# Optimization experiments

Measured on AMD Instinct MI355X. Metric: run time of the kernel, lower is better.

Reference implementation:

```python
import jax, jax.numpy as jnp
import numpy as np

B, T, C, H = 2, 2048, 1024, 16
HS = C // H  # head_size = 64
EPS = 1e-5


def setup_inputs() -> dict:
    key = jax.random.key(0)
    ks = jax.random.split(key, 12)
    s = 0.02
    return {
        "x": jax.random.normal(ks[0], (B, T, C), jnp.float32),
        # per-head q/k/v linears stacked on a leading head axis [H, C, HS]
        "Wq": jax.random.normal(ks[1], (H, C, HS), jnp.float32) * s,
        "bq": jnp.zeros((H, HS), jnp.float32),
        "Wk": jax.random.normal(ks[2], (H, C, HS), jnp.float32) * s,
        "bk": jnp.zeros((H, HS), jnp.float32),
        "Wv": jax.random.normal(ks[3], (H, C, HS), jnp.float32) * s,
        "bv": jnp.zeros((H, HS), jnp.float32),
        # output projection [H*HS, C] == [C, C]
        "Wo": jax.random.normal(ks[4], (C, C), jnp.float32) * s,
        "bo": jnp.zeros((C,), jnp.float32),
        # feed-forward: C -> 4C -> C
        "W1": jax.random.normal(ks[5], (C, 4 * C), jnp.float32) * s,
        "b1": jnp.zeros((4 * C,), jnp.float32),
        "W2": jax.random.normal(ks[6], (4 * C, C), jnp.float32) * s,
        "b2": jnp.zeros((C,), jnp.float32),
        # custom LayerNorm params (broadcast over last dim)
        "gamma1": jnp.ones((C,), jnp.float32),
        "beta1": jnp.zeros((C,), jnp.float32),
        "gamma2": jnp.ones((C,), jnp.float32),
        "beta2": jnp.zeros((C,), jnp.float32),
    }


def _ln(x, gamma, beta):
    # NOTE: faithful to the source: normalizes over axis=1 (the SEQUENCE axis
    # for [B,T,C] input), uses unbiased variance (torch default), and puts eps
    # OUTSIDE the sqrt: (x - mean) / (sqrt(var) + eps).
    mean = x.mean(axis=1, keepdims=True)
    var = x.var(axis=1, keepdims=True, ddof=1)
    return gamma * ((x - mean) / (jnp.sqrt(var) + EPS)) + beta


def reference(x, Wq, bq, Wk, bk, Wv, bv, Wo, bo, W1, b1, W2, b2,
              gamma1, beta1, gamma2, beta2):
    # --- self-attention sublayer (pre-norm, residual) ---
    h = _ln(x, gamma1, beta1)
    q = jnp.einsum('btc,hcd->bhtd', h, Wq) + bq[None, :, None, :]
    k = jnp.einsum('btc,hcd->bhtd', h, Wk) + bk[None, :, None, :]
    v = jnp.einsum('btc,hcd->bhtd', h, Wv) + bv[None, :, None, :]
    wei = jax.nn.softmax(jnp.einsum('bhtd,bhsd->bhts', q, k) * (HS ** -0.5), axis=-1)
    attn = jnp.einsum('bhts,bhsd->bhtd', wei, v)          # [B,H,T,HS]
    attn = attn.transpose(0, 2, 1, 3).reshape(B, T, H * HS)  # head-order concat
    x = x + attn @ Wo + bo
    # --- feed-forward sublayer (pre-norm, residual) ---
    h2 = _ln(x, gamma2, beta2)
    x = x + jax.nn.relu(h2 @ W1 + b1) @ W2 + b2
    return x
```

## Files before the change

kernel.cpp:

```cpp
#include <hip/hip_runtime.h>
#include <hip/hip_bf16.h>

#define Bq 2
#define Tq 2048
#define Cq 1024
#define Hq 16
#define HSq 64
#define EPSq 1e-5f

using bf16 = __hip_bfloat16;
using f32x4 = __attribute__((ext_vector_type(4))) float;
using f32x16 = __attribute__((ext_vector_type(16))) float;
using bf16x8 = __attribute__((ext_vector_type(8))) __bf16;

__device__ __forceinline__ bf16 f2bf(float f) { return __float2bfloat16(f); }
__device__ __forceinline__ unsigned short f2u(float f) {
    return __builtin_bit_cast(unsigned short, __float2bfloat16(f));
}
__device__ __forceinline__ void gload16(const void* g, void* l) {
    __builtin_amdgcn_global_load_lds((const __attribute__((address_space(1))) void*)g,
                                     (__attribute__((address_space(3))) void*)l, 16, 0, 0);
}

__global__ void k_transpose(const float* __restrict__ src, bf16* __restrict__ dst,
                            int R, int Cc, long strideSrc, long strideDst) {
    __shared__ bf16 tile[32][33];
    const long zb = blockIdx.z;
    src += zb * strideSrc;
    dst += zb * strideDst;
    int c0 = blockIdx.x * 32, r0 = blockIdx.y * 32;
    int tx = threadIdx.x & 31, ty = threadIdx.x >> 5;
    for (int i = ty; i < 32; i += 8)
        tile[i][tx] = f2bf(src[(long)(r0 + i) * Cc + (c0 + tx)]);
    __syncthreads();
    for (int i = ty; i < 32; i += 8)
        dst[(long)(c0 + i) * R + (r0 + tx)] = tile[tx][i];
}

__global__ void k_pack_bias(const float* __restrict__ a, const float* __restrict__ b,
                            const float* __restrict__ c, float* __restrict__ dst) {
    int i = blockIdx.x * 256 + threadIdx.x;
    dst[i] = a[i];
    dst[1024 + i] = b[i];
    dst[2048 + i] = c[i];
}

__global__ void k_ln_part(const float* __restrict__ x, float* __restrict__ ps,
                          float* __restrict__ pss) {
    int c = blockIdx.x * 256 + threadIdx.x;
    int b = blockIdx.y;
    int tc = blockIdx.z;
    const float* p = x + (long)b * Tq * Cq + (long)tc * 64 * Cq + c;
    float s = 0.f, ss = 0.f;
    for (int t = 0; t < 64; ++t) {
        float v = p[(long)t * Cq];
        s += v;
        ss += v * v;
    }
    long o = ((long)tc * Bq + b) * Cq + c;
    ps[o] = s;
    pss[o] = ss;
}

__global__ void k_ln_fin(const float* __restrict__ ps, const float* __restrict__ pss,
                         float* __restrict__ mean, float* __restrict__ rstd) {
    int i = blockIdx.x * 256 + threadIdx.x;
    float s = 0.f, ss = 0.f;
    for (int tc = 0; tc < 32; ++tc) {
        s += ps[(long)tc * (Bq * Cq) + i];
        ss += pss[(long)tc * (Bq * Cq) + i];
    }
    float m = s / (float)Tq;
    float var = (ss - s * m) / (float)(Tq - 1);
    var = fmaxf(var, 0.f);
    mean[i] = m;
    rstd[i] = 1.0f / (sqrtf(var) + EPSq);
}

__global__ void k_ln_apply(const float* __restrict__ x, const float* __restrict__ mean,
                           const float* __restrict__ rstd, const float* __restrict__ gamma,
                           const float* __restrict__ beta, bf16* __restrict__ out) {
    long i = (long)blockIdx.x * 256 + threadIdx.x;
    int c = (int)(i & (Cq - 1));
    long bt = i >> 10;
    int b = (int)(bt >> 11);
    float m = mean[b * Cq + c], r = rstd[b * Cq + c];
    out[i] = f2bf(gamma[c] * ((x[i] - m) * r) + beta[c]);
}

__device__ __forceinline__ void xcd_swizzle(int& bx, int& by) {
    const int gx = gridDim.x;
    const int nwg = gx * gridDim.y;
    const int bid = blockIdx.y * gx + blockIdx.x;
    const int swz = (bid & 7) * (nwg >> 3) + (bid >> 3);
    bx = swz % gx;
    by = swz / gx;
}

template <int MODE>
__global__ __launch_bounds__(256, 3) void k_gemm_nt(
    const bf16* __restrict__ A, int lda, const bf16* __restrict__ Bt, int ldb, int K,
    const float* __restrict__ bias, bf16* __restrict__ outB, int ldout) {
    __shared__ __bf16 sA[2][128 * 32];
    __shared__ __bf16 sB[2][128 * 32];
    int bx, by;
    xcd_swizzle(bx, by);
    const int m0 = by * 128, n0 = bx * 128;
    const int tid = threadIdx.x;
    const int lane = tid & 63, wave = tid >> 6;
    const int lane15 = lane & 15, quad = lane >> 4;
    const int wm = (wave >> 1) * 64, wn = (wave & 1) * 64;
    const int srow = wave * 16 + (lane >> 2);
    const int scol = (((lane & 3) ^ ((lane >> 3) & 3)) * 8);
    const int sq8 = (quad ^ ((lane15 >> 1) & 3)) * 8;
    __bf16* a00 = &sA[0][wave * 512];
    __bf16* a01 = &sA[0][2048 + wave * 512];
    __bf16* a10 = &sA[1][wave * 512];
    __bf16* a11 = &sA[1][2048 + wave * 512];
    __bf16* b00 = &sB[0][wave * 512];
    __bf16* b01 = &sB[0][2048 + wave * 512];
    __bf16* b10 = &sB[1][wave * 512];
    __bf16* b11 = &sB[1][2048 + wave * 512];
    const bf16* Ap = A + (long)(m0 + srow) * lda + scol;
    const bf16* Ap2 = Ap + 64L * lda;
    const bf16* Bp = Bt + (long)(n0 + srow) * ldb + scol;
    const bf16* Bp2 = Bp + 64L * ldb;

    f32x4 acc[4][4];
#pragma unroll
    for (int i = 0; i < 4; ++i)
#pragma unroll
        for (int j = 0; j < 4; ++j)
#pragma unroll
            for (int p = 0; p < 4; ++p) acc[i][j][p] = 0.f;

    for (int k0 = 0; k0 < K; k0 += 64) {
        __syncthreads();
        gload16(Ap + k0, a00);
        gload16(Ap2 + k0, a01);
        gload16(Ap + k0 + 32, a10);
        gload16(Ap2 + k0 + 32, a11);
        gload16(Bp + k0, b00);
        gload16(Bp2 + k0, b01);
        gload16(Bp + k0 + 32, b10);
        gload16(Bp2 + k0 + 32, b11);
        __syncthreads();
#pragma unroll
        for (int kk = 0; kk < 2; ++kk) {
            bf16x8 af[4], bfr[4];
#pragma unroll
            for (int i = 0; i < 4; ++i)
                af[i] = *(const bf16x8*)(&sA[kk][(wm + i * 16 + lane15) * 32 + sq8]);
#pragma unroll
            for (int j = 0; j < 4; ++j)
                bfr[j] = *(const bf16x8*)(&sB[kk][(wn + j * 16 + lane15) * 32 + sq8]);
#pragma unroll
            for (int i = 0; i < 4; ++i)
#pragma unroll
                for (int j = 0; j < 4; ++j)
                    acc[i][j] = __builtin_amdgcn_mfma_f32_16x16x32_bf16(af[i], bfr[j],
                                                                        acc[i][j], 0, 0, 0);
        }
    }
    if (MODE == 0) {
#pragma unroll
        for (int i = 0; i < 4; ++i) {
            const int mm = m0 + wm + i * 16 + quad * 4;
            const int b = mm >> 11, t4 = mm & (Tq - 1);
#pragma unroll
            for (int j = 0; j < 4; ++j) {
                const int n = n0 + wn + j * 16 + lane15;
                const int which = n >> 10, hh = (n >> 6) & (Hq - 1), d = n & (HSq - 1);
                const long bh = (long)b * Hq + hh;
                const float bb = bias[n];
                if (which == 0) {
#pragma unroll
                    for (int p = 0; p < 4; ++p)
                        outB[bh * 131072 + (long)(t4 + p) * HSq + d] =
                            f2bf((acc[i][j][p] + bb) * 0.125f);
                } else if (which == 1) {
#pragma unroll
                    for (int p = 0; p < 4; ++p)
                        outB[4194304L + bh * 131072 + (long)(t4 + p) * HSq + d] =
                            f2bf(acc[i][j][p] + bb);
                } else {
                    ushort4 pk;
                    pk.x = f2u(acc[i][j][0] + bb);
                    pk.y = f2u(acc[i][j][1] + bb);
                    pk.z = f2u(acc[i][j][2] + bb);
                    pk.w = f2u(acc[i][j][3] + bb);
                    *(ushort4*)(&outB[8388608L + bh * 131072 + (long)d * Tq + t4]) = pk;
                }
            }
        }
    } else {
#pragma unroll
        for (int i = 0; i < 4; ++i) {
#pragma unroll
            for (int p = 0; p < 4; ++p) {
                const int m = m0 + wm + i * 16 + quad * 4 + p;
#pragma unroll
                for (int j = 0; j < 4; ++j) {
                    const int n = n0 + wn + j * 16 + lane15;
                    outB[(long)m * ldout + n] = f2bf(fmaxf(acc[i][j][p] + bias[n], 0.f));
                }
            }
        }
    }
}

template <int MODE>
__global__ __launch_bounds__(256, 4) void k_gemm_n64(
    const bf16* __restrict__ A, int lda, const bf16* __restrict__ Bt, int ldb, int K,
    const float* __restrict__ bias, const float* __restrict__ residF,
    float* __restrict__ outF, int ldout) {
    __shared__ __bf16 sA[2][128 * 32];
    __shared__ __bf16 sB[2][64 * 32];
    int bx, by;
    xcd_swizzle(bx, by);
    const int m0 = by * 128, n0 = bx * 64;
    const int tid = threadIdx.x;
    const int lane = tid & 63, wave = tid >> 6;
    const int lane15 = lane & 15, quad = lane >> 4;
    const int wm = wave * 32;
    const int srow = wave * 16 + (lane >> 2);
    const int scol = (((lane & 3) ^ ((lane >> 3) & 3)) * 8);
    const int sq8 = (quad ^ ((lane15 >> 1) & 3)) * 8;
    __bf16* a00 = &sA[0][wave * 512];
    __bf16* a01 = &sA[0][2048 + wave * 512];
    __bf16* a10 = &sA[1][wave * 512];
    __bf16* a11 = &sA[1][2048 + wave * 512];
    __bf16* b00 = &sB[0][wave * 512];
    __bf16* b10 = &sB[1][wave * 512];
    const bf16* Ap = A + (long)(m0 + srow) * lda + scol;
    const bf16* Ap2 = Ap + 64L * lda;
    const bf16* Bp = Bt + (long)(n0 + srow) * ldb + scol;

    f32x4 acc[2][4];
#pragma unroll
    for (int i = 0; i < 2; ++i)
#pragma unroll
        for (int j = 0; j < 4; ++j)
#pragma unroll
            for (int p = 0; p < 4; ++p) acc[i][j][p] = 0.f;

    for (int k0 = 0; k0 < K; k0 += 64) {
        __syncthreads();
        gload16(Ap + k0, a00);
        gload16(Ap2 + k0, a01);
        gload16(Ap + k0 + 32, a10);
        gload16(Ap2 + k0 + 32, a11);
        gload16(Bp + k0, b00);
        gload16(Bp + k0 + 32, b10);
        __syncthreads();
#pragma unroll
        for (int kk = 0; kk < 2; ++kk) {
            bf16x8 af[2], bfr[4];
#pragma unroll
            for (int i = 0; i < 2; ++i)
                af[i] = *(const bf16x8*)(&sA[kk][(wm + i * 16 + lane15) * 32 + sq8]);
#pragma unroll
            for (int j = 0; j < 4; ++j)
                bfr[j] = *(const bf16x8*)(&sB[kk][(j * 16 + lane15) * 32 + sq8]);
#pragma unroll
            for (int i = 0; i < 2; ++i)
#pragma unroll
                for (int j = 0; j < 4; ++j)
                    acc[i][j] = __builtin_amdgcn_mfma_f32_16x16x32_bf16(af[i], bfr[j],
                                                                        acc[i][j], 0, 0, 0);
        }
    }
#pragma unroll
    for (int i = 0; i < 2; ++i) {
#pragma unroll
        for (int p = 0; p < 4; ++p) {
            const int m = m0 + wm + i * 16 + quad * 4 + p;
#pragma unroll
            for (int j = 0; j < 4; ++j) {
                const int n = n0 + j * 16 + lane15;
                outF[(long)m * ldout + n] =
                    acc[i][j][p] + bias[n] + residF[(long)m * ldout + n];
            }
        }
    }
}

__global__ __launch_bounds__(256, 2) void k_attn(const bf16* __restrict__ qkv,
                                                 bf16* __restrict__ attn) {
    __shared__ __bf16 sK[64 * 72];
    __shared__ __bf16 sVt[64 * 72];
    const int bh = blockIdx.y;
    const int q0 = blockIdx.x * 128;
    const int tid = threadIdx.x, wave = tid >> 6, lane = tid & 63;
    const int lane31 = lane & 31, laneh = lane >> 5;
    const bf16* Qp = qkv + (long)bh * 131072;
    const bf16* Kp = qkv + 4194304L + (long)bh * 131072;
    const bf16* Vtp = qkv + 8388608L + (long)bh * 131072;
    bf16x8 qa[4];
#pragma unroll
    for (int s = 0; s < 4; ++s)
        qa[s] = *(const bf16x8*)(&Qp[(long)(q0 + wave * 32 + lane31) * HSq + s * 16 + laneh * 8]);
    f32x16 o[2];
#pragma unroll
    for (int dt = 0; dt < 2; ++dt)
#pragma unroll
        for (int r = 0; r < 16; ++r) o[dt][r] = 0.f;
    float rs = 0.f;
    const int r0 = tid >> 3, c0 = (tid & 7) * 8;
    const int r1 = r0 + 32;

    uint4 nk0 = *(const uint4*)(&Kp[(long)r0 * HSq + c0]);
    uint4 nk1 = *(const uint4*)(&Kp[(long)r1 * HSq + c0]);
    uint4 nv0 = *(const uint4*)(&Vtp[(long)r0 * Tq + c0]);
    uint4 nv1 = *(const uint4*)(&Vtp[(long)r1 * Tq + c0]);

    for (int kc = 0; kc < Tq; kc += 64) {
        __syncthreads();
        *(uint4*)(&sK[r0 * 72 + c0]) = nk0;
        *(uint4*)(&sK[r1 * 72 + c0]) = nk1;
        *(uint4*)(&sVt[r0 * 72 + c0]) = nv0;
        *(uint4*)(&sVt[r1 * 72 + c0]) = nv1;
        __syncthreads();
        if (kc + 64 < Tq) {
            nk0 = *(const uint4*)(&Kp[(long)(kc + 64 + r0) * HSq + c0]);
            nk1 = *(const uint4*)(&Kp[(long)(kc + 64 + r1) * HSq + c0]);
            nv0 = *(const uint4*)(&Vtp[(long)r0 * Tq + kc + 64 + c0]);
            nv1 = *(const uint4*)(&Vtp[(long)r1 * Tq + kc + 64 + c0]);
        }
#pragma unroll
        for (int nt = 0; nt < 2; ++nt) {
            f32x16 z;
#pragma unroll
            for (int r = 0; r < 16; ++r) z[r] = 0.f;
            __builtin_amdgcn_s_setprio(1);
#pragma unroll
            for (int s = 0; s < 4; ++s) {
                bf16x8 kb =
                    *(const bf16x8*)(&sK[(nt * 32 + lane31) * 72 + s * 16 + laneh * 8]);
                z = __builtin_amdgcn_mfma_f32_32x32x16_bf16(kb, qa[s], z, 0, 0, 0);
            }
            __builtin_amdgcn_s_setprio(0);
            float e[16];
#pragma unroll
            for (int r = 0; r < 16; ++r) {
                e[r] = __expf(z[r]);
                rs += e[r];
            }
            unsigned int pk[8];
#pragma unroll
            for (int g = 0; g < 4; ++g)
#pragma unroll
                for (int h = 0; h < 2; ++h)
                    pk[g * 2 + h] = (unsigned int)f2u(e[g * 4 + 2 * h]) |
                                    ((unsigned int)f2u(e[g * 4 + 2 * h + 1]) << 16);
            unsigned int sa0 = laneh ? pk[0] : pk[2], sa1 = laneh ? pk[1] : pk[3];
            unsigned int ra0 = __shfl_xor((int)sa0, 32), ra1 = __shfl_xor((int)sa1, 32);
            unsigned int sb0 = laneh ? pk[4] : pk[6], sb1 = laneh ? pk[5] : pk[7];
            unsigned int rb0 = __shfl_xor((int)sb0, 32), rb1 = __shfl_xor((int)sb1, 32);
            uint4 f0, f1;
            if (laneh == 0) {
                f0 = {pk[0], pk[1], ra0, ra1};
                f1 = {pk[4], pk[5], rb0, rb1};
            } else {
                f0 = {ra0, ra1, pk[2], pk[3]};
                f1 = {rb0, rb1, pk[6], pk[7]};
            }
            bf16x8 pa0 = __builtin_bit_cast(bf16x8, f0);
            bf16x8 pa1 = __builtin_bit_cast(bf16x8, f1);
            __builtin_amdgcn_s_setprio(1);
#pragma unroll
            for (int dt = 0; dt < 2; ++dt) {
                bf16x8 vb0 =
                    *(const bf16x8*)(&sVt[(dt * 32 + lane31) * 72 + nt * 32 + laneh * 8]);
                bf16x8 vb1 = *(const bf16x8*)(&sVt[(dt * 32 + lane31) * 72 + nt * 32 + 16 +
                                                   laneh * 8]);
                o[dt] = __builtin_amdgcn_mfma_f32_32x32x16_bf16(pa0, vb0, o[dt], 0, 0, 0);
                o[dt] = __builtin_amdgcn_mfma_f32_32x32x16_bf16(pa1, vb1, o[dt], 0, 0, 0);
            }
            __builtin_amdgcn_s_setprio(0);
        }
    }
    float ltot = rs + __shfl_xor(rs, 32);
    float linv = 1.0f / ltot;
    const int b = bh >> 4, hh = bh & 15;
#pragma unroll
    for (int r = 0; r < 16; ++r) {
        const int tl = (r & 3) + 8 * (r >> 2) + 4 * laneh;
        float inv = __shfl(linv, tl);
        const int t = q0 + wave * 32 + tl;
        const long base = ((long)b * Tq + t) * Cq + hh * HSq;
#pragma unroll
        for (int dt = 0; dt < 2; ++dt)
            attn[base + dt * 32 + lane31] = f2bf(o[dt][r] * inv);
    }
}

extern "C" void kernel_launch(void* const* d_in, const int* in_sizes, int n_in,
                              void* d_out, int out_size, void* d_ws, size_t ws_size,
                              hipStream_t stream) {
    const float* x = (const float*)d_in[0];
    const float* Wq = (const float*)d_in[1];
    const float* bqv = (const float*)d_in[2];
    const float* Wk = (const float*)d_in[3];
    const float* bkv = (const float*)d_in[4];
    const float* Wv = (const float*)d_in[5];
    const float* bvv = (const float*)d_in[6];
    const float* Wo = (const float*)d_in[7];
    const float* bo = (const float*)d_in[8];
    const float* W1 = (const float*)d_in[9];
    const float* b1 = (const float*)d_in[10];
    const float* W2 = (const float*)d_in[11];
    const float* b2 = (const float*)d_in[12];
    const float* g1 = (const float*)d_in[13];
    const float* be1 = (const float*)d_in[14];
    const float* g2 = (const float*)d_in[15];
    const float* be2 = (const float*)d_in[16];

    char* ws = (char*)d_ws;
    size_t off = 0;
    auto alloc = [&](size_t bytes) {
        void* p = ws + off;
        off += (bytes + 255) & ~(size_t)255;
        return p;
    };
    bf16* regA = (bf16*)alloc(32L * 1024 * 1024);
    float* x2 = (float*)alloc(4096L * 1024 * 4);
    bf16* buf1 = (bf16*)alloc(4096L * 1024 * 2);
    float* bqkv = (float*)alloc(3072L * 4);
    float* ps = (float*)alloc(32L * Bq * Cq * 4);
    float* pss = (float*)alloc(32L * Bq * Cq * 4);
    float* mean1 = (float*)alloc(Bq * Cq * 4);
    float* rstd1 = (float*)alloc(Bq * Cq * 4);
    float* mean2 = (float*)alloc(Bq * Cq * 4);
    float* rstd2 = (float*)alloc(Bq * Cq * 4);
    bf16* dres = (bf16*)d_out;
    float* outF = (float*)d_out;

    k_ln_part<<<dim3(4, Bq, 32), 256, 0, stream>>>(x, ps, pss);
    k_ln_fin<<<dim3(8), 256, 0, stream>>>(ps, pss, mean1, rstd1);
    k_ln_apply<<<dim3(16384), 256, 0, stream>>>(x, mean1, rstd1, g1, be1, dres);

    k_transpose<<<dim3(2, 32, 16), 256, 0, stream>>>(Wq, buf1, 1024, 64, 65536, 65536);
    k_transpose<<<dim3(2, 32, 16), 256, 0, stream>>>(Wk, buf1 + 1048576, 1024, 64, 65536, 65536);
    k_transpose<<<dim3(2, 32, 16), 256, 0, stream>>>(Wv, buf1 + 2097152, 1024, 64, 65536, 65536);
    k_pack_bias<<<dim3(4), 256, 0, stream>>>(bqv, bkv, bvv, bqkv);
    k_gemm_nt<0><<<dim3(24, 32), 256, 0, stream>>>(dres, 1024, buf1, 1024, 1024, bqkv, regA, 0);
    k_attn<<<dim3(16, 32), 256, 0, stream>>>(regA, dres);
    k_transpose<<<dim3(32, 32, 1), 256, 0, stream>>>(Wo, buf1, 1024, 1024, 0, 0);
    k_gemm_n64<1><<<dim3(16, 32), 256, 0, stream>>>(dres, 1024, buf1, 1024, 1024, bo, x, x2,
                                                    1024);
    k_ln_part<<<dim3(4, Bq, 32), 256, 0, stream>>>(x2, ps, pss);
    k_ln_fin<<<dim3(8), 256, 0, stream>>>(ps, pss, mean2, rstd2);
    k_ln_apply<<<dim3(16384), 256, 0, stream>>>(x2, mean2, rstd2, g2, be2, dres);

    k_transpose<<<dim3(128, 32, 1), 256, 0, stream>>>(W1, buf1, 1024, 4096, 0, 0);
    k_gemm_nt<2><<<dim3(32, 32), 256, 0, stream>>>(dres, 1024, buf1, 1024, 1024, b1, regA, 4096);
    k_transpose<<<dim3(32, 128, 1), 256, 0, stream>>>(W2, buf1, 4096, 1024, 0, 0);
    k_gemm_n64<3><<<dim3(16, 32), 256, 0, stream>>>(regA, 4096, buf1, 4096, 4096, b2, x2, outF,
                                                    1024);
}
```

Before: 392.6 us.

## Split attention over key halves with a combine kernel; merge QKV weight transposes

The attention kernel now splits the key sequence into two halves along a new grid z dimension. Each half writes unnormalized fp32 partial outputs and row sums to scratch buffers (x2, d_out, ps, pss), and a new combine kernel sums them, normalizes and writes bf16 into a regA region. This doubles the block count and raises launch bounds to 4 waves per SIMD to improve occupancy, at the cost of extra fp32 round-trip traffic and one more launch. The three Q/K/V weight transposes and the bias pack are fused into one launch to cut launch overhead.

```diff
diff --git a/kernel.cpp b/kernel.cpp
--- a/kernel.cpp
+++ b/kernel.cpp
@@ -37,12 +37,26 @@
         dst[(long)(c0 + i) * R + (r0 + tx)] = tile[tx][i];
 }
 
-__global__ void k_pack_bias(const float* __restrict__ a, const float* __restrict__ b,
-                            const float* __restrict__ c, float* __restrict__ dst) {
-    int i = blockIdx.x * 256 + threadIdx.x;
-    dst[i] = a[i];
-    dst[1024 + i] = b[i];
-    dst[2048 + i] = c[i];
+__global__ void k_transpose3(const float* __restrict__ Wq, const float* __restrict__ Wk,
+                             const float* __restrict__ Wv, const float* __restrict__ bqv,
+                             const float* __restrict__ bkv, const float* __restrict__ bvv,
+                             bf16* __restrict__ dst, float* __restrict__ bdst) {
+    __shared__ bf16 tile[32][33];
+    const int zb = blockIdx.z;
+    const int which = zb >> 4, head = zb & 15;
+    const float* src = (which == 0 ? Wq : which == 1 ? Wk : Wv) + (long)head * 65536;
+    bf16* d = dst + (long)which * 1048576 + (long)head * 65536;
+    int c0 = blockIdx.x * 32, r0 = blockIdx.y * 32;
+    int tx = threadIdx.x & 31, ty = threadIdx.x >> 5;
+    for (int i = ty; i < 32; i += 8)
+        tile[i][tx] = f2bf(src[(long)(r0 + i) * 64 + (c0 + tx)]);
+    if (blockIdx.x == 0 && blockIdx.y == 0 && zb < 12) {
+        int i = zb * 256 + threadIdx.x;
+        bdst[i] = i < 1024 ? bqv[i] : i < 2048 ? bkv[i - 1024] : bvv[i - 2048];
+    }
+    __syncthreads();
+    for (int i = ty; i < 32; i += 8)
+        d[(long)(c0 + i) * 1024 + (r0 + tx)] = tile[tx][i];
 }
 
 __global__ void k_ln_part(const float* __restrict__ x, float* __restrict__ ps,
@@ -285,12 +299,19 @@
     }
 }
 
-__global__ __launch_bounds__(256, 2) void k_attn(const bf16* __restrict__ qkv,
-                                                 bf16* __restrict__ attn) {
+__global__ __launch_bounds__(256, 4) void k_attn(const bf16* __restrict__ qkv,
+                                                 float* __restrict__ po0,
+                                                 float* __restrict__ po1,
+                                                 float* __restrict__ rs0,
+                                                 float* __restrict__ rs1) {
     __shared__ __bf16 sK[64 * 72];
     __shared__ __bf16 sVt[64 * 72];
     const int bh = blockIdx.y;
     const int q0 = blockIdx.x * 128;
+    const int z = blockIdx.z;
+    const int kc0 = z << 10;
+    float* __restrict__ po = z ? po1 : po0;
+    float* __restrict__ rsb = z ? rs1 : rs0;
     const int tid = threadIdx.x, wave = tid >> 6, lane = tid & 63;
     const int lane31 = lane & 31, laneh = lane >> 5;
     const bf16* Qp = qkv + (long)bh * 131072;
@@ -309,19 +330,19 @@
     const int r0 = tid >> 3, c0 = (tid & 7) * 8;
     const int r1 = r0 + 32;
 
-    uint4 nk0 = *(const uint4*)(&Kp[(long)r0 * HSq + c0]);
-    uint4 nk1 = *(const uint4*)(&Kp[(long)r1 * HSq + c0]);
-    uint4 nv0 = *(const uint4*)(&Vtp[(long)r0 * Tq + c0]);
-    uint4 nv1 = *(const uint4*)(&Vtp[(long)r1 * Tq + c0]);
-
-    for (int kc = 0; kc < Tq; kc += 64) {
+    uint4 nk0 = *(const uint4*)(&Kp[(long)(kc0 + r0) * HSq + c0]);
+    uint4 nk1 = *(const uint4*)(&Kp[(long)(kc0 + r1) * HSq + c0]);
+    uint4 nv0 = *(const uint4*)(&Vtp[(long)r0 * Tq + kc0 + c0]);
+    uint4 nv1 = *(const uint4*)(&Vtp[(long)r1 * Tq + kc0 + c0]);
+
+    for (int kc = kc0; kc < kc0 + 1024; kc += 64) {
         __syncthreads();
         *(uint4*)(&sK[r0 * 72 + c0]) = nk0;
         *(uint4*)(&sK[r1 * 72 + c0]) = nk1;
         *(uint4*)(&sVt[r0 * 72 + c0]) = nv0;
         *(uint4*)(&sVt[r1 * 72 + c0]) = nv1;
         __syncthreads();
-        if (kc + 64 < Tq) {
+        if (kc + 64 < kc0 + 1024) {
             nk0 = *(const uint4*)(&Kp[(long)(kc + 64 + r0) * HSq + c0]);
             nk1 = *(const uint4*)(&Kp[(long)(kc + 64 + r1) * HSq + c0]);
             nv0 = *(const uint4*)(&Vtp[(long)r0 * Tq + kc + 64 + c0]);
@@ -329,21 +350,21 @@
         }
 #pragma unroll
         for (int nt = 0; nt < 2; ++nt) {
-            f32x16 z;
-#pragma unroll
-            for (int r = 0; r < 16; ++r) z[r] = 0.f;
+            f32x16 zz;
+#pragma unroll
+            for (int r = 0; r < 16; ++r) zz[r] = 0.f;
             __builtin_amdgcn_s_setprio(1);
 #pragma unroll
             for (int s = 0; s < 4; ++s) {
                 bf16x8 kb =
                     *(const bf16x8*)(&sK[(nt * 32 + lane31) * 72 + s * 16 + laneh * 8]);
-                z = __builtin_amdgcn_mfma_f32_32x32x16_bf16(kb, qa[s], z, 0, 0, 0);
+                zz = __builtin_amdgcn_mfma_f32_32x32x16_bf16(kb, qa[s], zz, 0, 0, 0);
             }
             __builtin_amdgcn_s_setprio(0);
             float e[16];
 #pragma unroll
             for (int r = 0; r < 16; ++r) {
-                e[r] = __expf(z[r]);
+                e[r] = __expf(zz[r]);
                 rs += e[r];
             }
             unsigned int pk[8];
@@ -381,18 +402,35 @@
         }
     }
     float ltot = rs + __shfl_xor(rs, 32);
-    float linv = 1.0f / ltot;
-    const int b = bh >> 4, hh = bh & 15;
+    if (laneh == 0) rsb[(bh << 11) + q0 + wave * 32 + lane31] = ltot;
 #pragma unroll
     for (int r = 0; r < 16; ++r) {
         const int tl = (r & 3) + 8 * (r >> 2) + 4 * laneh;
-        float inv = __shfl(linv, tl);
         const int t = q0 + wave * 32 + tl;
-        const long base = ((long)b * Tq + t) * Cq + hh * HSq;
-#pragma unroll
-        for (int dt = 0; dt < 2; ++dt)
-            attn[base + dt * 32 + lane31] = f2bf(o[dt][r] * inv);
-    }
+        float* pb = po + ((long)(bh << 11) + t) * 64;
+#pragma unroll
+        for (int dt = 0; dt < 2; ++dt) pb[dt * 32 + lane31] = o[dt][r];
+    }
+}
+
+__global__ __launch_bounds__(256) void k_attn_combine(
+    const float* __restrict__ po0, const float* __restrict__ po1,
+    const float* __restrict__ rs0, const float* __restrict__ rs1,
+    bf16* __restrict__ out) {
+    const long i = ((long)blockIdx.x * 256 + threadIdx.x) * 4;
+    const int d = (int)(i & 63);
+    const long qq = i >> 6;
+    const int bh = (int)(qq >> 11), t = (int)(qq & 2047);
+    const float inv = 1.0f / (rs0[qq] + rs1[qq]);
+    const f32x4 a = *(const f32x4*)(po0 + i);
+    const f32x4 b = *(const f32x4*)(po1 + i);
+    const int bb = bh >> 4, hh = bh & 15;
+    ushort4 pk;
+    pk.x = f2u((a[0] + b[0]) * inv);
+    pk.y = f2u((a[1] + b[1]) * inv);
+    pk.z = f2u((a[2] + b[2]) * inv);
+    pk.w = f2u((a[3] + b[3]) * inv);
+    *(ushort4*)(&out[(((long)bb * Tq + t) << 10) + hh * 64 + d]) = pk;
 }
 
 extern "C" void kernel_launch(void* const* d_in, const int* in_sizes, int n_in,
@@ -435,20 +473,20 @@
     float* rstd2 = (float*)alloc(Bq * Cq * 4);
     bf16* dres = (bf16*)d_out;
     float* outF = (float*)d_out;
+    float* po1 = (float*)d_out;
+    bf16* attn_out = regA + 12582912;
 
     k_ln_part<<<dim3(4, Bq, 32), 256, 0, stream>>>(x, ps, pss);
     k_ln_fin<<<dim3(8), 256, 0, stream>>>(ps, pss, mean1, rstd1);
     k_ln_apply<<<dim3(16384), 256, 0, stream>>>(x, mean1, rstd1, g1, be1, dres);
 
-    k_transpose<<<dim3(2, 32, 16), 256, 0, stream>>>(Wq, buf1, 1024, 64, 65536, 65536);
-    k_transpose<<<dim3(2, 32, 16), 256, 0, stream>>>(Wk, buf1 + 1048576, 1024, 64, 65536, 65536);
-    k_transpose<<<dim3(2, 32, 16), 256, 0, stream>>>(Wv, buf1 + 2097152, 1024, 64, 65536, 65536);
-    k_pack_bias<<<dim3(4), 256, 0, stream>>>(bqv, bkv, bvv, bqkv);
+    k_transpose3<<<dim3(2, 32, 48), 256, 0, stream>>>(Wq, Wk, Wv, bqv, bkv, bvv, buf1, bqkv);
     k_gemm_nt<0><<<dim3(24, 32), 256, 0, stream>>>(dres, 1024, buf1, 1024, 1024, bqkv, regA, 0);
-    k_attn<<<dim3(16, 32), 256, 0, stream>>>(regA, dres);
+    k_attn<<<dim3(16, 32, 2), 256, 0, stream>>>(regA, x2, po1, ps, pss);
+    k_attn_combine<<<dim3(4096), 256, 0, stream>>>(x2, po1, ps, pss, attn_out);
     k_transpose<<<dim3(32, 32, 1), 256, 0, stream>>>(Wo, buf1, 1024, 1024, 0, 0);
-    k_gemm_n64<1><<<dim3(16, 32), 256, 0, stream>>>(dres, 1024, buf1, 1024, 1024, bo, x, x2,
-                                                    1024);
+    k_gemm_n64<1><<<dim3(16, 32), 256, 0, stream>>>(attn_out, 1024, buf1, 1024, 1024, bo, x,
+                                                    x2, 1024);
     k_ln_part<<<dim3(4, Bq, 32), 256, 0, stream>>>(x2, ps, pss);
     k_ln_fin<<<dim3(8), 256, 0, stream>>>(ps, pss, mean2, rstd2);
     k_ln_apply<<<dim3(16384), 256, 0, stream>>>(x2, mean2, rstd2, g2, be2, dres);
```

New measurement: 389.0 us. Within noise of the previous version (-0.9%).
